# Optimization experiments

Measured on AMD Instinct MI355X. Metric: run time of the kernel, lower is better.

The kernel has to match this reference:

```python
import jax, jax.numpy as jnp
import numpy as np
from functools import partial

N_NODES = 20000
N_EDGES = 640000
IN_C = 64
HID = 256
OUT_C = 64
HIST = 12
HORIZON = 6


def gcn_conv(x, w, b, src, dst, deg_inv, norm):
    # PyG GCNConv with self loops: out = D^-1/2 (A+I) D^-1/2 (x @ w) + b
    xw = x @ w                                   # [N, H]
    agg = jax.ops.segment_sum(xw[src] * norm[:, None], dst, num_segments=N_NODES)
    return agg + xw * deg_inv[:, None] + b


def gru_cell(x, h, wih, whh, bih, bhh):
    # torch.nn.GRUCell semantics; wih: [3H, in], whh: [3H, H]
    gi = x @ wih.T + bih
    gh = h @ whh.T + bhh
    ir, iz, inn = jnp.split(gi, 3, axis=-1)
    hr, hz, hn = jnp.split(gh, 3, axis=-1)
    r = jax.nn.sigmoid(ir + hr)
    z = jax.nn.sigmoid(iz + hz)
    n = jnp.tanh(inn + r * hn)
    return (1.0 - z) * n + z * h


def setup_inputs() -> dict:
    key = jax.random.key(0)
    ks = jax.random.split(key, 20)
    s = lambda fan: 1.0 / np.sqrt(fan)
    inp = {
        "x_seq": jax.random.normal(ks[0], (1, HIST, N_NODES, IN_C), dtype=jnp.float32),
        "src": jax.random.randint(ks[1], (N_EDGES,), 0, N_NODES),
        "dst": jax.random.randint(ks[2], (N_EDGES,), 0, N_NODES),
        "gcn1_w": jax.random.normal(ks[3], (IN_C, HID), jnp.float32) * s(IN_C),
        "gcn1_b": jnp.zeros((HID,), jnp.float32),
        "gcn2_w": jax.random.normal(ks[4], (HID, HID), jnp.float32) * s(HID),
        "gcn2_b": jnp.zeros((HID,), jnp.float32),
        "proj_w": jax.random.normal(ks[5], (HID, OUT_C), jnp.float32) * s(HID),
        "proj_b": jnp.zeros((OUT_C,), jnp.float32),
    }
    for i, name in enumerate(["gru1", "gru2", "gru3"]):
        k1, k2 = jax.random.split(ks[6 + i])
        inp[f"{name}_wih"] = jax.random.normal(k1, (3 * HID, HID), jnp.float32) * s(HID)
        inp[f"{name}_whh"] = jax.random.normal(k2, (3 * HID, HID), jnp.float32) * s(HID)
        inp[f"{name}_bih"] = jnp.zeros((3 * HID,), jnp.float32)
        inp[f"{name}_bhh"] = jnp.zeros((3 * HID,), jnp.float32)
    return inp


def reference(x_seq, src, dst, gcn1_w, gcn1_b, gcn2_w, gcn2_b, proj_w, proj_b,
              gru1_wih, gru1_whh, gru1_bih, gru1_bhh,
              gru2_wih, gru2_whh, gru2_bih, gru2_bhh,
              gru3_wih, gru3_whh, gru3_bih, gru3_bhh):
    # symmetric GCN normalization with self loops (static graph -> compute once)
    deg = jax.ops.segment_sum(jnp.ones((N_EDGES,), jnp.float32), dst, num_segments=N_NODES) + 1.0
    deg_is = deg ** -0.5
    norm = deg_is[src] * deg_is[dst]   # per-edge norm
    deg_inv = 1.0 / deg                # self-loop norm

    def cell(xt, h1, h2, h3):
        x = jax.nn.relu(gcn_conv(xt, gcn1_w, gcn1_b, src, dst, deg_inv, norm))
        x = jax.nn.relu(gcn_conv(x, gcn2_w, gcn2_b, src, dst, deg_inv, norm))
        h1 = gru_cell(x, h1, gru1_wih, gru1_whh, gru1_bih, gru1_bhh)
        h2 = gru_cell(h1, h2, gru2_wih, gru2_whh, gru2_bih, gru2_bhh)
        h3 = gru_cell(h2, h3, gru3_wih, gru3_whh, gru3_bih, gru3_bhh)
        return h1, h2, h3

    h0 = jnp.zeros((N_NODES, HID), jnp.float32)

    def enc_step(carry, xt):
        return cell(xt, *carry), None

    (h1, h2, h3), _ = jax.lax.scan(enc_step, (h0, h0, h0), x_seq[0])  # [T,N,C]

    def dec_step(carry, _):
        h1, h2, h3, xd = carry
        h1, h2, h3 = cell(xd, h1, h2, h3)
        y = h3 @ proj_w + proj_b       # [N, OUT_C]
        return (h1, h2, h3, y), y

    _, ys = jax.lax.scan(dec_step, (h1, h2, h3, x_seq[0, -1]), None, length=HORIZON)
    return ys[None]  # [1, HORIZON, N, OUT_C]
```

## Files before the change

### kernel.cpp

```cpp
#include <hip/hip_runtime.h>

#define N_NODESC 20000
#define N_EDGESC 640000

typedef _Float16 f16;
typedef __attribute__((ext_vector_type(4))) _Float16 f16x4;
typedef __attribute__((ext_vector_type(8))) _Float16 f16x8;
typedef __attribute__((ext_vector_type(4))) float f32x4;

__device__ __forceinline__ f32x4 mfma16(f16x8 a, f16x8 b, f32x4 c){
  return __builtin_amdgcn_mfma_f32_16x16x32_f16(a, b, c, 0, 0, 0);
}
__device__ __forceinline__ float sigm(float x){ return 1.f/(1.f+__expf(-x)); }
__device__ __forceinline__ float tanh_(float x){
  x = fminf(fmaxf(x, -15.f), 15.f);
  float e = __expf(-2.f*x);
  return (1.f - e)/(1.f + e);
}
__device__ __forceinline__ void stage16(const void* g, void* l){
  __builtin_amdgcn_global_load_lds((const __attribute__((address_space(1))) unsigned int*)g,
                                   (__attribute__((address_space(3))) unsigned int*)l, 16, 0, 0);
}
#define SB       __builtin_amdgcn_sched_barrier(0)
#define AS_VM(n) do{ asm volatile("s_waitcnt vmcnt(" #n ")" ::: "memory"); SB; }while(0)
#define BAR      do{ __builtin_amdgcn_s_barrier(); SB; }while(0)

__global__ __launch_bounds__(256) void k_hist(const int* __restrict__ dst, int* __restrict__ cnt){
  int e = blockIdx.x*256 + threadIdx.x;
  if(e < N_EDGESC) atomicAdd(&cnt[dst[e]], 1);
}

__global__ __launch_bounds__(1024) void k_scan(const int* __restrict__ cnt, int* __restrict__ row_ptr,
    float* __restrict__ deg_inv, float* __restrict__ deg_is){
  __shared__ int wsum[16];
  int t = threadIdx.x;
  int base = t*20;
  int loc[20]; int s = 0;
  #pragma unroll
  for(int i=0;i<20;i++){ int idx=base+i; int v = (idx<N_NODESC)? cnt[idx] : 0; loc[i]=s; s+=v; }
  int lane = t&63, wv = t>>6;
  int incl = s;
  #pragma unroll
  for(int off=1; off<64; off<<=1){ int u = __shfl_up(incl, off); if(lane>=off) incl += u; }
  if(lane==63) wsum[wv]=incl;
  __syncthreads();
  int woff=0;
  for(int i=0;i<wv;i++) woff += wsum[i];
  int excl = woff + incl - s;
  #pragma unroll
  for(int i=0;i<20;i++){
    int idx=base+i;
    if(idx<N_NODESC){
      row_ptr[idx] = excl + loc[i];
      float d = (float)(cnt[idx]+1);
      deg_inv[idx] = 1.f/d;
      deg_is[idx]  = rsqrtf(d);
    }
  }
  if(t==1023) row_ptr[N_NODESC] = woff + incl;
}

__global__ __launch_bounds__(256) void k_fill(const int* __restrict__ src, const int* __restrict__ dst,
    const int* __restrict__ row_ptr, int* __restrict__ cursor, const float* __restrict__ deg_is,
    int2* __restrict__ ev){
  int e = blockIdx.x*256 + threadIdx.x;
  if(e >= N_EDGESC) return;
  int d = dst[e], s = src[e];
  int p = atomicAdd(&cursor[d], 1);
  int2 v;
  v.x = s;
  v.y = __float_as_int(deg_is[s]*deg_is[d]);
  ev[row_ptr[d] + p] = v;
}

__global__ __launch_bounds__(256) void k_cvt(const float* __restrict__ x, f16* __restrict__ o, int n4){
  int i = blockIdx.x*256 + threadIdx.x;
  if(i >= n4) return;
  f32x4 v = *(const f32x4*)(x + (size_t)i*4);
  *(f16x4*)(o + (size_t)i*4) = __builtin_convertvector(v, f16x4);
}

__global__ __launch_bounds__(256) void k_pack(const float* __restrict__ w, f16* __restrict__ dstp,
    int K, int NO, int trans){
  int t = blockIdx.x*256 + threadIdx.x;
  if(t >= K*NO) return;
  int i = t&7, g = (t>>3)&3, rest = t>>5;
  int c = rest % NO, kb = rest / NO;
  int k = kb*32 + g*8 + i;
  float v = trans ? w[(size_t)c*K + k] : w[(size_t)k*NO + c];
  dstp[t] = (f16)v;
}

__global__ __launch_bounds__(256) void k_agg64(const f16* __restrict__ x,
    const int* __restrict__ row_ptr, const int2* __restrict__ ev,
    const float* __restrict__ deg_inv, f16* __restrict__ O){
  int n = (blockIdx.x*256 + threadIdx.x)>>6;
  int c = threadIdx.x&63;
  if(n >= N_NODESC) return;
  float acc = deg_inv[n]*(float)x[(size_t)n*64 + c];
  int e0 = row_ptr[n], e1 = row_ptr[n+1];
  int e = e0;
  for(; e+4<=e1; e+=4){
    int2 a=ev[e], b=ev[e+1], cc=ev[e+2], d=ev[e+3];
    float v0=(float)x[(size_t)a.x*64+c],  v1=(float)x[(size_t)b.x*64+c];
    float v2=(float)x[(size_t)cc.x*64+c], v3=(float)x[(size_t)d.x*64+c];
    acc += __int_as_float(a.y)*v0 + __int_as_float(b.y)*v1
         + __int_as_float(cc.y)*v2 + __int_as_float(d.y)*v3;
  }
  for(; e<e1; e++){ int2 a=ev[e]; acc += __int_as_float(a.y)*(float)x[(size_t)a.x*64+c]; }
  O[(size_t)n*64+c] = (f16)acc;
}

__global__ __launch_bounds__(256) void k_agg256(const f16* __restrict__ x1,
    const int* __restrict__ row_ptr, const int2* __restrict__ ev,
    const float* __restrict__ deg_inv, f16* __restrict__ O){
  int n = (blockIdx.x*256 + threadIdx.x)>>6;
  int lane = threadIdx.x&63;
  if(n >= N_NODESC) return;
  const f16x4* xv = (const f16x4*)x1;
  f32x4 acc = __builtin_convertvector(xv[(size_t)n*64 + lane], f32x4) * deg_inv[n];
  int e0 = row_ptr[n], e1 = row_ptr[n+1];
  int e = e0;
  for(; e+4<=e1; e+=4){
    int2 a=ev[e], b=ev[e+1], cc=ev[e+2], d=ev[e+3];
    f32x4 v0=__builtin_convertvector(xv[(size_t)a.x*64+lane],  f32x4);
    f32x4 v1=__builtin_convertvector(xv[(size_t)b.x*64+lane],  f32x4);
    f32x4 v2=__builtin_convertvector(xv[(size_t)cc.x*64+lane], f32x4);
    f32x4 v3=__builtin_convertvector(xv[(size_t)d.x*64+lane],  f32x4);
    acc += v0*__int_as_float(a.y); acc += v1*__int_as_float(b.y);
    acc += v2*__int_as_float(cc.y); acc += v3*__int_as_float(d.y);
  }
  for(; e<e1; e++){ int2 a=ev[e];
    acc += __builtin_convertvector(xv[(size_t)a.x*64+lane], f32x4)*__int_as_float(a.y); }
  ((f16x4*)O)[(size_t)n*64+lane] = __builtin_convertvector(acc, f16x4);
}

__global__ __launch_bounds__(256) void k_gcn1(const f16* __restrict__ A,
    const f16* __restrict__ Bp, const float* __restrict__ bias, f16* __restrict__ C){
  __shared__ f16x8 ldsv[512];
  char* lds = (char*)ldsv;
  const int tid = threadIdx.x, lane = tid&63, w = tid>>6, l15 = lane&15, q = lane>>4;
  const int m0 = blockIdx.x*64;
  int rg = m0 + lane; if(rg > N_NODESC-1) rg = N_NODESC-1;
  #pragma unroll
  for(int i=0;i<2;i++){
    int region = i*4 + w;
    int kbb = region>>2, qq = region&3;
    stage16((const char*)A + (size_t)rg*128 + kbb*64 + qq*16, lds + region*1024 + lane*16);
  }
  AS_VM(0);
  BAR;
  f32x4 acc[4][4];
  #pragma unroll
  for(int rt=0;rt<4;rt++)
    #pragma unroll
    for(int ct=0;ct<4;ct++) acc[rt][ct] = (f32x4){0.f,0.f,0.f,0.f};
  #pragma unroll
  for(int kb=0;kb<2;kb++){
    f16x8 bf[4];
    #pragma unroll
    for(int ct=0;ct<4;ct++){
      int c = w*64 + ct*16 + l15;
      bf[ct] = *(const f16x8*)(Bp + ((unsigned)(kb*256 + c)*4 + q)*8);
    }
    #pragma unroll
    for(int rt=0;rt<4;rt++){
      f16x8 ah = *(const f16x8*)(lds + (kb*4+q)*1024 + (rt*16+l15)*16);
      #pragma unroll
      for(int ct=0;ct<4;ct++)
        acc[rt][ct] = mfma16(ah, bf[ct], acc[rt][ct]);
    }
  }
  #pragma unroll
  for(int rt=0;rt<4;rt++)
    #pragma unroll
    for(int ct=0;ct<4;ct++){
      int c = w*64 + ct*16 + l15;
      float bv = bias[c];
      #pragma unroll
      for(int j=0;j<4;j++){
        int r = m0 + rt*16 + q*4 + j;
        if(r < N_NODESC) C[(size_t)r*256 + c] = (f16)fmaxf(acc[rt][ct][j] + bv, 0.f);
      }
    }
}

__global__ __launch_bounds__(256,2) void k_gcn2(const f16* __restrict__ A,
    const f16* __restrict__ Bp, const float* __restrict__ bias, f16* __restrict__ C){
  __shared__ f16x8 ldsv[1024];
  char* lds = (char*)ldsv;
  const int tid = threadIdx.x, lane = tid&63, w = tid>>6, l15 = lane&15, q = lane>>4;
  const int m0 = blockIdx.x*64;
  int rg = m0 + lane; if(rg > N_NODESC-1) rg = N_NODESC-1;
  const size_t abyte = (size_t)rg*512;
  f32x4 acc[4][4];
  #pragma unroll
  for(int rt=0;rt<4;rt++)
    #pragma unroll
    for(int ct=0;ct<4;ct++) acc[rt][ct] = (f32x4){0.f,0.f,0.f,0.f};
  f16x8 bf[2][4];
  stage16((const char*)A + abyte + w*16, lds + 0*4096 + w*1024 + lane*16);
  SB;
  stage16((const char*)A + abyte + 64 + w*16, lds + 1*4096 + w*1024 + lane*16);
  SB;
  #pragma unroll
  for(int ct=0;ct<4;ct++){
    int c = w*64 + ct*16 + l15;
    bf[0][ct] = *(const f16x8*)(Bp + ((unsigned)(0*256 + c)*4 + q)*8);
  }
  SB;
  #pragma unroll
  for(int kb=0;kb<8;kb++){
    const int cur = kb&3, rB = kb&1;
    if(kb<6){
      stage16((const char*)A + abyte + (kb+2)*64 + w*16, lds + ((kb+2)&3)*4096 + w*1024 + lane*16);
      SB;
    }
    if(kb<7){
      #pragma unroll
      for(int ct=0;ct<4;ct++){
        int c = w*64 + ct*16 + l15;
        bf[rB^1][ct] = *(const f16x8*)(Bp + ((unsigned)((kb+1)*256 + c)*4 + q)*8);
      }
      SB;
    }
    if(kb<6){ AS_VM(5); } else if(kb==6){ AS_VM(4); } else { AS_VM(0); }
    BAR;
    #pragma unroll
    for(int rt=0;rt<4;rt++){
      f16x8 ah = *(const f16x8*)(lds + cur*4096 + q*1024 + (rt*16+l15)*16);
      #pragma unroll
      for(int ct=0;ct<4;ct++)
        acc[rt][ct] = mfma16(ah, bf[rB][ct], acc[rt][ct]);
    }
  }
  #pragma unroll
  for(int rt=0;rt<4;rt++)
    #pragma unroll
    for(int ct=0;ct<4;ct++){
      int c = w*64 + ct*16 + l15;
      float bv = bias[c];
      #pragma unroll
      for(int j=0;j<4;j++){
        int r = m0 + rt*16 + q*4 + j;
        if(r < N_NODESC) C[(size_t)r*256 + c] = (f16)fmaxf(acc[rt][ct][j] + bv, 0.f);
      }
    }
}

__global__ __launch_bounds__(256,2) void k_gru(
    const f16* __restrict__ X, const f16* __restrict__ H, f16* __restrict__ Nh,
    const f16* __restrict__ Wi, const f16* __restrict__ Wh,
    const float* __restrict__ bih, const float* __restrict__ bhh){
  __shared__ f16x8 ldsv[2048];
  char* lds = (char*)ldsv;
  const int NB = 1252, QQ = NB>>3, RR = NB&7;
  int bid = blockIdx.x;
  int xcd = bid & 7, jj = bid >> 3;
  int nid = (xcd < RR) ? xcd*(QQ+1) + jj : RR*(QQ+1) + (xcd-RR)*QQ + jj;
  const int m0 = (nid>>2)*64;
  const int cb = nid&3;
  const int tid = threadIdx.x, lane = tid&63, w = tid>>6, l15 = lane&15, q = lane>>4;
  const int cc = cb*64 + w*16 + l15;
  int rg = m0 + lane; if(rg > N_NODESC-1) rg = N_NODESC-1;
  const size_t abyte = (size_t)rg*512;
  const f16* pl[2] = {X, H};
  f32x4 acc[6][4];
  #pragma unroll
  for(int m=0;m<6;m++)
    #pragma unroll
    for(int rt=0;rt<4;rt++) acc[m][rt] = (f32x4){0.f,0.f,0.f,0.f};
  const unsigned wbase = (unsigned)cc*32 + q*8;
  f16x8 breg[2][6];
  #pragma unroll
  for(int i=0;i<2;i++){
    int pc = w*2 + i; int p = pc>>2, c = pc&3;
    stage16((const char*)pl[p] + abyte + c*16, lds + 0*8192 + p*4096 + c*1024 + lane*16);
  }
  SB;
  #pragma unroll
  for(int i=0;i<2;i++){
    int pc = w*2 + i; int p = pc>>2, c = pc&3;
    stage16((const char*)pl[p] + abyte + 64 + c*16, lds + 1*8192 + p*4096 + c*1024 + lane*16);
  }
  SB;
  {
    breg[0][0] = *(const f16x8*)(Wi + wbase);
    breg[0][1] = *(const f16x8*)(Wi + wbase + 8192);
    breg[0][2] = *(const f16x8*)(Wi + wbase + 16384);
    breg[0][3] = *(const f16x8*)(Wh + wbase);
    breg[0][4] = *(const f16x8*)(Wh + wbase + 8192);
    breg[0][5] = *(const f16x8*)(Wh + wbase + 16384);
  }
  SB;
  #pragma unroll
  for(int kb=0;kb<8;kb++){
    const int cur = kb&3, rB = kb&1;
    if(kb<6){
      #pragma unroll
      for(int i=0;i<2;i++){
        int pc = w*2 + i; int p = pc>>2, c = pc&3;
        stage16((const char*)pl[p] + abyte + (kb+2)*64 + c*16,
                lds + ((kb+2)&3)*8192 + p*4096 + c*1024 + lane*16);
      }
      SB;
    }
    if(kb<7){
      unsigned wo = wbase + (unsigned)(kb+1)*24576u;
      breg[rB^1][0] = *(const f16x8*)(Wi + wo);
      breg[rB^1][1] = *(const f16x8*)(Wi + wo + 8192);
      breg[rB^1][2] = *(const f16x8*)(Wi + wo + 16384);
      breg[rB^1][3] = *(const f16x8*)(Wh + wo);
      breg[rB^1][4] = *(const f16x8*)(Wh + wo + 8192);
      breg[rB^1][5] = *(const f16x8*)(Wh + wo + 16384);
      SB;
    }
    if(kb<6){ AS_VM(8); } else if(kb==6){ AS_VM(6); } else { AS_VM(0); }
    BAR;
    #pragma unroll
    for(int rt=0;rt<4;rt++){
      const int ro = cur*8192 + q*1024 + (rt*16+l15)*16;
      f16x8 ax = *(const f16x8*)(lds + ro);
      f16x8 ah = *(const f16x8*)(lds + 4096 + ro);
      acc[0][rt] = mfma16(ax, breg[rB][0], acc[0][rt]);
      acc[1][rt] = mfma16(ax, breg[rB][1], acc[1][rt]);
      acc[2][rt] = mfma16(ax, breg[rB][2], acc[2][rt]);
      acc[3][rt] = mfma16(ah, breg[rB][3], acc[3][rt]);
      acc[4][rt] = mfma16(ah, breg[rB][4], acc[4][rt]);
      acc[5][rt] = mfma16(ah, breg[rB][5], acc[5][rt]);
    }
  }
  float bir=bih[cc], biz=bih[cc+256], bin=bih[cc+512];
  float bhr=bhh[cc], bhz=bhh[cc+256], bhn=bhh[cc+512];
  #pragma unroll
  for(int rt=0;rt<4;rt++){
    #pragma unroll
    for(int j=0;j<4;j++){
      int r = m0 + rt*16 + q*4 + j;
      if(r < N_NODESC){
        float ir=acc[0][rt][j], iz=acc[1][rt][j], in_=acc[2][rt][j];
        float hr=acc[3][rt][j], hz=acc[4][rt][j], hn=acc[5][rt][j];
        float rgt = sigm(ir+bir + hr+bhr);
        float zg = sigm(iz+biz + hz+bhz);
        float ng = tanh_(in_+bin + rgt*(hn+bhn));
        float ho = (float)H[(size_t)r*256 + cc];
        float v = (1.f-zg)*ng + zg*ho;
        Nh[(size_t)r*256 + cc] = (f16)v;
      }
    }
  }
}

__global__ __launch_bounds__(256,2) void k_proj(const f16* __restrict__ A,
    const f16* __restrict__ Bp, const float* __restrict__ bias,
    float* __restrict__ C, f16* __restrict__ Cf16){
  __shared__ f16x8 ldsv[1024];
  char* lds = (char*)ldsv;
  const int tid = threadIdx.x, lane = tid&63, w = tid>>6, l15 = lane&15, q = lane>>4;
  const int m0 = blockIdx.x*64;
  const int cc = w*16 + l15;
  int rg = m0 + lane; if(rg > N_NODESC-1) rg = N_NODESC-1;
  const size_t abyte = (size_t)rg*512;
  f32x4 acc[4];
  #pragma unroll
  for(int rt=0;rt<4;rt++) acc[rt] = (f32x4){0.f,0.f,0.f,0.f};
  f16x8 bf[2];
  stage16((const char*)A + abyte + w*16, lds + 0*4096 + w*1024 + lane*16);
  SB;
  stage16((const char*)A + abyte + 64 + w*16, lds + 1*4096 + w*1024 + lane*16);
  SB;
  bf[0] = *(const f16x8*)(Bp + ((unsigned)(0*64 + cc)*4 + q)*8);
  SB;
  #pragma unroll
  for(int kb=0;kb<8;kb++){
    const int cur = kb&3, rB = kb&1;
    if(kb<6){
      stage16((const char*)A + abyte + (kb+2)*64 + w*16, lds + ((kb+2)&3)*4096 + w*1024 + lane*16);
      SB;
    }
    if(kb<7){
      bf[rB^1] = *(const f16x8*)(Bp + ((unsigned)((kb+1)*64 + cc)*4 + q)*8);
      SB;
    }
    if(kb<6){ AS_VM(2); } else if(kb==6){ AS_VM(1); } else { AS_VM(0); }
    BAR;
    #pragma unroll
    for(int rt=0;rt<4;rt++){
      f16x8 ah = *(const f16x8*)(lds + cur*4096 + q*1024 + (rt*16+l15)*16);
      acc[rt] = mfma16(ah, bf[rB], acc[rt]);
    }
  }
  #pragma unroll
  for(int rt=0;rt<4;rt++){
    float bv = bias[cc];
    #pragma unroll
    for(int j=0;j<4;j++){
      int r = m0 + rt*16 + q*4 + j;
      if(r < N_NODESC){
        float v = acc[rt][j] + bv;
        C[(size_t)r*64 + cc] = v;
        Cf16[(size_t)r*64 + cc] = (f16)v;
      }
    }
  }
}

extern "C" void kernel_launch(void* const* d_in, const int* in_sizes, int n_in,
                              void* d_out, int out_size, void* d_ws, size_t ws_size,
                              hipStream_t stream){
  const float* x_seq  = (const float*)d_in[0];
  const int*   srcp   = (const int*)  d_in[1];
  const int*   dstp   = (const int*)  d_in[2];
  const float* gcn1_w = (const float*)d_in[3];
  const float* gcn1_b = (const float*)d_in[4];
  const float* gcn2_w = (const float*)d_in[5];
  const float* gcn2_b = (const float*)d_in[6];
  const float* proj_w = (const float*)d_in[7];
  const float* proj_b = (const float*)d_in[8];
  const float* wih[3] = {(const float*)d_in[9],  (const float*)d_in[13], (const float*)d_in[17]};
  const float* whh[3] = {(const float*)d_in[10], (const float*)d_in[14], (const float*)d_in[18]};
  const float* bih[3] = {(const float*)d_in[11], (const float*)d_in[15], (const float*)d_in[19]};
  const float* bhh[3] = {(const float*)d_in[12], (const float*)d_in[16], (const float*)d_in[20]};
  float* out = (float*)d_out;

  const size_t NP = (size_t)N_NODESC*256;
  char* p = (char*)d_ws;
  auto alloc = [&](size_t bytes)->char*{ char* r = p; p += (bytes + 255) & ~(size_t)255; return r; };
  int*   deg_cnt = (int*)  alloc((size_t)2*N_NODESC*4);
  int*   cursor  = deg_cnt + N_NODESC;
  int*   row_ptr = (int*)  alloc((size_t)(N_NODESC+1)*4);
  float* deg_inv = (float*)alloc((size_t)N_NODESC*4);
  float* deg_is  = (float*)alloc((size_t)N_NODESC*4);
  int2*  ev      = (int2*) alloc((size_t)N_EDGESC*8);
  f16* xf16 = (f16*)alloc((size_t)12*N_NODESC*64*2);
  f16* xdec = (f16*)alloc((size_t)N_NODESC*64*2);
  f16* z64  = (f16*)alloc((size_t)N_NODESC*64*2);
  f16* x1   = (f16*)alloc(NP*2);
  f16* xa   = (f16*)alloc(NP*2);
  f16* hbuf = (f16*)alloc((size_t)2*3*NP*2);
  f16* pk_gcn1 = (f16*)alloc((size_t)64*256*2);
  f16* pk_gcn2 = (f16*)alloc((size_t)256*256*2);
  f16* pk_proj = (f16*)alloc((size_t)256*64*2);
  f16* pk_wi[3]; f16* pk_wh[3];
  for(int i=0;i<3;i++){ pk_wi[i]=(f16*)alloc((size_t)256*768*2); pk_wh[i]=(f16*)alloc((size_t)256*768*2); }

  hipMemsetAsync(deg_cnt, 0, (size_t)2*N_NODESC*4, stream);
  hipMemsetAsync(hbuf,    0, (size_t)3*NP*2, stream);

  k_hist<<<2500,256,0,stream>>>(dstp, deg_cnt);
  k_scan<<<1,1024,0,stream>>>(deg_cnt, row_ptr, deg_inv, deg_is);
  k_fill<<<2500,256,0,stream>>>(srcp, dstp, row_ptr, cursor, deg_is, ev);
  k_cvt<<<15000,256,0,stream>>>(x_seq, xf16, 12*N_NODESC*64/4);

  k_pack<<<64, 256,0,stream>>>(gcn1_w, pk_gcn1, 64, 256, 0);
  k_pack<<<256,256,0,stream>>>(gcn2_w, pk_gcn2, 256,256, 0);
  k_pack<<<64, 256,0,stream>>>(proj_w, pk_proj, 256, 64, 0);
  for(int i=0;i<3;i++){
    k_pack<<<768,256,0,stream>>>(wih[i], pk_wi[i], 256, 768, 1);
    k_pack<<<768,256,0,stream>>>(whh[i], pk_wh[i], 256, 768, 1);
  }

  auto Hs = [&](int slot, int g)->f16*{ return hbuf + ((size_t)(slot*3+g))*NP; };

  for(int s=0; s<18; s++){
    const f16* xt;
    if(s < 12)       xt = xf16 + (size_t)s*N_NODESC*64;
    else if(s == 12) xt = xf16 + (size_t)11*N_NODESC*64;
    else             xt = xdec;
    int cur = s&1, nxt = cur^1;

    k_agg64 <<<5000,256,0,stream>>>(xt, row_ptr, ev, deg_inv, z64);
    k_gcn1  <<<313, 256,0,stream>>>(z64, pk_gcn1, gcn1_b, x1);
    k_agg256<<<5000,256,0,stream>>>(x1, row_ptr, ev, deg_inv, xa);
    k_gcn2  <<<313, 256,0,stream>>>(xa, pk_gcn2, gcn2_b, xa);

    k_gru<<<1252,256,0,stream>>>(xa,        Hs(cur,0), Hs(nxt,0), pk_wi[0], pk_wh[0], bih[0], bhh[0]);
    k_gru<<<1252,256,0,stream>>>(Hs(nxt,0), Hs(cur,1), Hs(nxt,1), pk_wi[1], pk_wh[1], bih[1], bhh[1]);
    k_gru<<<1252,256,0,stream>>>(Hs(nxt,1), Hs(cur,2), Hs(nxt,2), pk_wi[2], pk_wh[2], bih[2], bhh[2]);

    if(s >= 12)
      k_proj<<<313,256,0,stream>>>(Hs(nxt,2), pk_proj, proj_b, out + (size_t)(s-12)*N_NODESC*64, xdec);
  }
}
```

Baseline: 3.805 ms.

## Preload full A tiles into LDS in GEMM kernels and parallelize degree scan

The single-block degree scan becomes a three-kernel multi-block scan (per-block scan, block-offset scan, fixup that also computes the degree norms). The GCN2, GRU and projection GEMM kernels stop using the 4-stage rolling LDS pipeline with per-step waits and barriers. They now stage the whole 64-row A tile (both X and H for the GRU) into LDS up front, then run the MFMA loop with no barriers. This removes per-iteration synchronization but doubles or quadruples LDS use per block and exposes the full load latency before any compute, which may cut occupancy for the GRU kernel; the gcn2 and proj launch bounds are raised to ask for more resident blocks.

```diff
diff --git a/kernel.cpp b/kernel.cpp
--- a/kernel.cpp
+++ b/kernel.cpp
@@ -30,34 +30,51 @@
   if(e < N_EDGESC) atomicAdd(&cnt[dst[e]], 1);
 }
 
-__global__ __launch_bounds__(1024) void k_scan(const int* __restrict__ cnt, int* __restrict__ row_ptr,
+__global__ __launch_bounds__(256) void k_scanA(const int* __restrict__ cnt,
+    int* __restrict__ row_ptr, int* __restrict__ btot){
+  __shared__ int ws[4];
+  int b = blockIdx.x, t = threadIdx.x;
+  int i = b*256 + t;
+  int v = (i < N_NODESC) ? cnt[i] : 0;
+  int lane = t&63, wv = t>>6;
+  int incl = v;
+  #pragma unroll
+  for(int off=1; off<64; off<<=1){ int u = __shfl_up(incl, off); if(lane>=off) incl += u; }
+  if(lane==63) ws[wv] = incl;
+  __syncthreads();
+  int woff = 0;
+  for(int k=0;k<wv;k++) woff += ws[k];
+  if(i < N_NODESC) row_ptr[i] = woff + incl - v;
+  if(t == 255) btot[b] = woff + incl;
+}
+
+__global__ __launch_bounds__(128) void k_scanB(const int* __restrict__ btot,
+    int* __restrict__ boff, int* __restrict__ row_ptr){
+  __shared__ int s[128];
+  int t = threadIdx.x;
+  int orig = (t < 79) ? btot[t] : 0;
+  s[t] = orig;
+  __syncthreads();
+  #pragma unroll
+  for(int off=1; off<128; off<<=1){
+    int u = (t>=off) ? s[t-off] : 0;
+    __syncthreads();
+    s[t] += u;
+    __syncthreads();
+  }
+  if(t < 79) boff[t] = s[t] - orig;
+  if(t == 0) row_ptr[N_NODESC] = N_EDGESC;
+}
+
+__global__ __launch_bounds__(256) void k_scanC(const int* __restrict__ cnt,
+    const int* __restrict__ boff, int* __restrict__ row_ptr,
     float* __restrict__ deg_inv, float* __restrict__ deg_is){
-  __shared__ int wsum[16];
-  int t = threadIdx.x;
-  int base = t*20;
-  int loc[20]; int s = 0;
-  #pragma unroll
-  for(int i=0;i<20;i++){ int idx=base+i; int v = (idx<N_NODESC)? cnt[idx] : 0; loc[i]=s; s+=v; }
-  int lane = t&63, wv = t>>6;
-  int incl = s;
-  #pragma unroll
-  for(int off=1; off<64; off<<=1){ int u = __shfl_up(incl, off); if(lane>=off) incl += u; }
-  if(lane==63) wsum[wv]=incl;
-  __syncthreads();
-  int woff=0;
-  for(int i=0;i<wv;i++) woff += wsum[i];
-  int excl = woff + incl - s;
-  #pragma unroll
-  for(int i=0;i<20;i++){
-    int idx=base+i;
-    if(idx<N_NODESC){
-      row_ptr[idx] = excl + loc[i];
-      float d = (float)(cnt[idx]+1);
-      deg_inv[idx] = 1.f/d;
-      deg_is[idx]  = rsqrtf(d);
-    }
-  }
-  if(t==1023) row_ptr[N_NODESC] = woff + incl;
+  int i = blockIdx.x*256 + threadIdx.x;
+  if(i >= N_NODESC) return;
+  row_ptr[i] += boff[blockIdx.x];
+  float d = (float)(cnt[i] + 1);
+  deg_inv[i] = 1.f/d;
+  deg_is[i]  = rsqrtf(d);
 }
 
 __global__ __launch_bounds__(256) void k_fill(const int* __restrict__ src, const int* __restrict__ dst,
@@ -185,50 +202,43 @@
     }
 }
 
-__global__ __launch_bounds__(256,2) void k_gcn2(const f16* __restrict__ A,
+__global__ __launch_bounds__(256,3) void k_gcn2(const f16* __restrict__ A,
     const f16* __restrict__ Bp, const float* __restrict__ bias, f16* __restrict__ C){
-  __shared__ f16x8 ldsv[1024];
+  __shared__ f16x8 ldsv[2048];
   char* lds = (char*)ldsv;
   const int tid = threadIdx.x, lane = tid&63, w = tid>>6, l15 = lane&15, q = lane>>4;
   const int m0 = blockIdx.x*64;
   int rg = m0 + lane; if(rg > N_NODESC-1) rg = N_NODESC-1;
   const size_t abyte = (size_t)rg*512;
+  #pragma unroll
+  for(int kb=0;kb<8;kb++)
+    stage16((const char*)A + abyte + kb*64 + w*16, lds + kb*4096 + w*1024 + lane*16);
+  AS_VM(0);
+  BAR;
   f32x4 acc[4][4];
   #pragma unroll
   for(int rt=0;rt<4;rt++)
     #pragma unroll
     for(int ct=0;ct<4;ct++) acc[rt][ct] = (f32x4){0.f,0.f,0.f,0.f};
   f16x8 bf[2][4];
-  stage16((const char*)A + abyte + w*16, lds + 0*4096 + w*1024 + lane*16);
-  SB;
-  stage16((const char*)A + abyte + 64 + w*16, lds + 1*4096 + w*1024 + lane*16);
-  SB;
   #pragma unroll
   for(int ct=0;ct<4;ct++){
     int c = w*64 + ct*16 + l15;
     bf[0][ct] = *(const f16x8*)(Bp + ((unsigned)(0*256 + c)*4 + q)*8);
   }
-  SB;
   #pragma unroll
   for(int kb=0;kb<8;kb++){
-    const int cur = kb&3, rB = kb&1;
-    if(kb<6){
-      stage16((const char*)A + abyte + (kb+2)*64 + w*16, lds + ((kb+2)&3)*4096 + w*1024 + lane*16);
-      SB;
-    }
+    const int rB = kb&1;
     if(kb<7){
       #pragma unroll
       for(int ct=0;ct<4;ct++){
         int c = w*64 + ct*16 + l15;
         bf[rB^1][ct] = *(const f16x8*)(Bp + ((unsigned)((kb+1)*256 + c)*4 + q)*8);
       }
-      SB;
-    }
-    if(kb<6){ AS_VM(5); } else if(kb==6){ AS_VM(4); } else { AS_VM(0); }
-    BAR;
+    }
     #pragma unroll
     for(int rt=0;rt<4;rt++){
-      f16x8 ah = *(const f16x8*)(lds + cur*4096 + q*1024 + (rt*16+l15)*16);
+      f16x8 ah = *(const f16x8*)(lds + kb*4096 + q*1024 + (rt*16+l15)*16);
       #pragma unroll
       for(int ct=0;ct<4;ct++)
         acc[rt][ct] = mfma16(ah, bf[rB][ct], acc[rt][ct]);
@@ -252,7 +262,7 @@
     const f16* __restrict__ X, const f16* __restrict__ H, f16* __restrict__ Nh,
     const f16* __restrict__ Wi, const f16* __restrict__ Wh,
     const float* __restrict__ bih, const float* __restrict__ bhh){
-  __shared__ f16x8 ldsv[2048];
+  __shared__ f16x8 ldsv[4096];
   char* lds = (char*)ldsv;
   const int NB = 1252, QQ = NB>>3, RR = NB&7;
   int bid = blockIdx.x;
@@ -265,6 +275,14 @@
   int rg = m0 + lane; if(rg > N_NODESC-1) rg = N_NODESC-1;
   const size_t abyte = (size_t)rg*512;
   const f16* pl[2] = {X, H};
+  #pragma unroll
+  for(int p=0;p<2;p++)
+    #pragma unroll
+    for(int kb=0;kb<8;kb++)
+      stage16((const char*)pl[p] + abyte + kb*64 + w*16,
+              lds + p*32768 + kb*4096 + w*1024 + lane*16);
+  AS_VM(0);
+  BAR;
   f32x4 acc[6][4];
   #pragma unroll
   for(int m=0;m<6;m++)
@@ -272,18 +290,6 @@
     for(int rt=0;rt<4;rt++) acc[m][rt] = (f32x4){0.f,0.f,0.f,0.f};
   const unsigned wbase = (unsigned)cc*32 + q*8;
   f16x8 breg[2][6];
-  #pragma unroll
-  for(int i=0;i<2;i++){
-    int pc = w*2 + i; int p = pc>>2, c = pc&3;
-    stage16((const char*)pl[p] + abyte + c*16, lds + 0*8192 + p*4096 + c*1024 + lane*16);
-  }
-  SB;
-  #pragma unroll
-  for(int i=0;i<2;i++){
-    int pc = w*2 + i; int p = pc>>2, c = pc&3;
-    stage16((const char*)pl[p] + abyte + 64 + c*16, lds + 1*8192 + p*4096 + c*1024 + lane*16);
-  }
-  SB;
   {
     breg[0][0] = *(const f16x8*)(Wi + wbase);
     breg[0][1] = *(const f16x8*)(Wi + wbase + 8192);
@@ -292,19 +298,9 @@
     breg[0][4] = *(const f16x8*)(Wh + wbase + 8192);
     breg[0][5] = *(const f16x8*)(Wh + wbase + 16384);
   }
-  SB;
   #pragma unroll
   for(int kb=0;kb<8;kb++){
-    const int cur = kb&3, rB = kb&1;
-    if(kb<6){
-      #pragma unroll
-      for(int i=0;i<2;i++){
-        int pc = w*2 + i; int p = pc>>2, c = pc&3;
-        stage16((const char*)pl[p] + abyte + (kb+2)*64 + c*16,
-                lds + ((kb+2)&3)*8192 + p*4096 + c*1024 + lane*16);
-      }
-      SB;
-    }
+    const int rB = kb&1;
     if(kb<7){
       unsigned wo = wbase + (unsigned)(kb+1)*24576u;
       breg[rB^1][0] = *(const f16x8*)(Wi + wo);
@@ -313,15 +309,12 @@
       breg[rB^1][3] = *(const f16x8*)(Wh + wo);
       breg[rB^1][4] = *(const f16x8*)(Wh + wo + 8192);
       breg[rB^1][5] = *(const f16x8*)(Wh + wo + 16384);
-      SB;
-    }
-    if(kb<6){ AS_VM(8); } else if(kb==6){ AS_VM(6); } else { AS_VM(0); }
-    BAR;
+    }
     #pragma unroll
     for(int rt=0;rt<4;rt++){
-      const int ro = cur*8192 + q*1024 + (rt*16+l15)*16;
+      const int ro = kb*4096 + q*1024 + (rt*16+l15)*16;
       f16x8 ax = *(const f16x8*)(lds + ro);
-      f16x8 ah = *(const f16x8*)(lds + 4096 + ro);
+      f16x8 ah = *(const f16x8*)(lds + 32768 + ro);
       acc[0][rt] = mfma16(ax, breg[rB][0], acc[0][rt]);
       acc[1][rt] = mfma16(ax, breg[rB][1], acc[1][rt]);
       acc[2][rt] = mfma16(ax, breg[rB][2], acc[2][rt]);
@@ -351,42 +344,34 @@
   }
 }
 
-__global__ __launch_bounds__(256,2) void k_proj(const f16* __restrict__ A,
+__global__ __launch_bounds__(256,4) void k_proj(const f16* __restrict__ A,
     const f16* __restrict__ Bp, const float* __restrict__ bias,
     float* __restrict__ C, f16* __restrict__ Cf16){
-  __shared__ f16x8 ldsv[1024];
+  __shared__ f16x8 ldsv[2048];
   char* lds = (char*)ldsv;
   const int tid = threadIdx.x, lane = tid&63, w = tid>>6, l15 = lane&15, q = lane>>4;
   const int m0 = blockIdx.x*64;
   const int cc = w*16 + l15;
   int rg = m0 + lane; if(rg > N_NODESC-1) rg = N_NODESC-1;
   const size_t abyte = (size_t)rg*512;
+  #pragma unroll
+  for(int kb=0;kb<8;kb++)
+    stage16((const char*)A + abyte + kb*64 + w*16, lds + kb*4096 + w*1024 + lane*16);
+  AS_VM(0);
+  BAR;
   f32x4 acc[4];
   #pragma unroll
   for(int rt=0;rt<4;rt++) acc[rt] = (f32x4){0.f,0.f,0.f,0.f};
   f16x8 bf[2];
-  stage16((const char*)A + abyte + w*16, lds + 0*4096 + w*1024 + lane*16);
-  SB;
-  stage16((const char*)A + abyte + 64 + w*16, lds + 1*4096 + w*1024 + lane*16);
-  SB;
   bf[0] = *(const f16x8*)(Bp + ((unsigned)(0*64 + cc)*4 + q)*8);
-  SB;
   #pragma unroll
   for(int kb=0;kb<8;kb++){
-    const int cur = kb&3, rB = kb&1;
-    if(kb<6){
-      stage16((const char*)A + abyte + (kb+2)*64 + w*16, lds + ((kb+2)&3)*4096 + w*1024 + lane*16);
-      SB;
-    }
-    if(kb<7){
+    const int rB = kb&1;
+    if(kb<7)
       bf[rB^1] = *(const f16x8*)(Bp + ((unsigned)((kb+1)*64 + cc)*4 + q)*8);
-      SB;
-    }
-    if(kb<6){ AS_VM(2); } else if(kb==6){ AS_VM(1); } else { AS_VM(0); }
-    BAR;
     #pragma unroll
     for(int rt=0;rt<4;rt++){
-      f16x8 ah = *(const f16x8*)(lds + cur*4096 + q*1024 + (rt*16+l15)*16);
+      f16x8 ah = *(const f16x8*)(lds + kb*4096 + q*1024 + (rt*16+l15)*16);
       acc[rt] = mfma16(ah, bf[rB], acc[rt]);
     }
   }
@@ -431,6 +416,8 @@
   int*   row_ptr = (int*)  alloc((size_t)(N_NODESC+1)*4);
   float* deg_inv = (float*)alloc((size_t)N_NODESC*4);
   float* deg_is  = (float*)alloc((size_t)N_NODESC*4);
+  int*   btot    = (int*)  alloc((size_t)128*4);
+  int*   boff    = (int*)  alloc((size_t)128*4);
   int2*  ev      = (int2*) alloc((size_t)N_EDGESC*8);
   f16* xf16 = (f16*)alloc((size_t)12*N_NODESC*64*2);
   f16* xdec = (f16*)alloc((size_t)N_NODESC*64*2);
@@ -447,10 +434,12 @@
   hipMemsetAsync(deg_cnt, 0, (size_t)2*N_NODESC*4, stream);
   hipMemsetAsync(hbuf,    0, (size_t)3*NP*2, stream);
 
-  k_hist<<<2500,256,0,stream>>>(dstp, deg_cnt);
-  k_scan<<<1,1024,0,stream>>>(deg_cnt, row_ptr, deg_inv, deg_is);
-  k_fill<<<2500,256,0,stream>>>(srcp, dstp, row_ptr, cursor, deg_is, ev);
-  k_cvt<<<15000,256,0,stream>>>(x_seq, xf16, 12*N_NODESC*64/4);
+  k_hist <<<2500,256,0,stream>>>(dstp, deg_cnt);
+  k_scanA<<<79,  256,0,stream>>>(deg_cnt, row_ptr, btot);
+  k_scanB<<<1,   128,0,stream>>>(btot, boff, row_ptr);
+  k_scanC<<<79,  256,0,stream>>>(deg_cnt, boff, row_ptr, deg_inv, deg_is);
+  k_fill <<<2500,256,0,stream>>>(srcp, dstp, row_ptr, cursor, deg_is, ev);
+  k_cvt  <<<15000,256,0,stream>>>(x_seq, xf16, 12*N_NODESC*64/4);
 
   k_pack<<<64, 256,0,stream>>>(gcn1_w, pk_gcn1, 64, 256, 0);
   k_pack<<<256,256,0,stream>>>(gcn2_w, pk_gcn2, 256,256, 0);
```

Result: no change. 3.787 ms (-0.5%).
